# Performance work log

Hardware: AMD Instinct MI355X
Metric: run time of the kernel (lower is better)

The kernel has to match this reference:

```python
import jax, jax.numpy as jnp
import numpy as np

B, S, H, NH = 8, 2048, 128, 4
HS = H // NH
EPS = 1e-8


def setup_inputs() -> dict:
    key = jax.random.key(0)
    ks = jax.random.split(key, 20)
    sc = 1.0 / np.sqrt(H)
    d = {
        'item_embeds': jax.random.normal(ks[0], (B, S, H), jnp.float32),
        'behavior_embeds': jax.random.normal(ks[1], (B, S, H), jnp.float32),
        'attn_mask': jnp.zeros((B, 1, S, S), jnp.float32),
    }
    names = ['Wq', 'Wk', 'Wv', 'Wqb', 'Wkb', 'Wvb', 'Wf']
    for i, n in enumerate(names):
        d[n] = jax.random.normal(ks[2 + i], (H, H), jnp.float32) * sc
        d['b' + n[1:]] = jnp.zeros((H,), jnp.float32)
    d['ln_w'] = jnp.ones((H,), jnp.float32)
    d['ln_b'] = jnp.zeros((H,), jnp.float32)
    return d


def _split_heads(x):
    # [B,S,H] -> [B,NH,S,HS]
    return x.reshape(B, S, NH, HS).transpose(0, 2, 1, 3)


def _layer_norm(x, w, b):
    u = jnp.mean(x, -1, keepdims=True)
    s = jnp.mean((x - u) ** 2, -1, keepdims=True)
    return w * ((x - u) / jnp.sqrt(s + EPS)) + b


def reference(item_embeds, behavior_embeds, attn_mask,
              Wq, bq, Wk, bk, Wv, bv,
              Wqb, bqb, Wkb, bkb, Wvb, bvb,
              Wf, bf, ln_w, ln_b):
    Q = _split_heads(item_embeds @ Wq + bq)
    K = _split_heads(item_embeds @ Wk + bk)
    V = _split_heads(item_embeds @ Wv + bv)
    Qb = _split_heads(behavior_embeds @ Wqb + bqb)
    Kb = _split_heads(behavior_embeds @ Wkb + bkb)
    # V_behavior computed in the original forward but unused downstream
    _Vb = _split_heads(behavior_embeds @ Wvb + bvb)
    scores = (jnp.einsum('bhqd,bhkd->bhqk', Q, K)
              + jnp.einsum('bhqd,bhkd->bhqk', Qb, Kb)) / np.sqrt(HS)
    scores = scores + attn_mask
    probs = jax.nn.softmax(scores, axis=-1)
    attn_out = jnp.einsum('bhqk,bhkd->bhqd', probs, V)
    attn_out = attn_out.transpose(0, 2, 1, 3).reshape(B, S, H)
    out = attn_out @ Wf + bf
    return _layer_norm(out + item_embeds, ln_w, ln_b)
```

## Files before the change

### kernel.cpp

```cpp
#include <hip/hip_runtime.h>
#include <math.h>

typedef unsigned short ushort_t;
typedef __attribute__((ext_vector_type(8))) short bf16x8;
typedef __attribute__((ext_vector_type(4))) float f32x4;

namespace {
constexpr int B = 8, S = 2048, H = 128, NH = 4, HS = 32;
constexpr float EPS = 1e-8f;
constexpr float SCALE = 0.17677669529663687f;
constexpr int QT = 16, KT = 64;
constexpr int NE = B * S * H;
constexpr int NML = B * NH * S;
}

__device__ __forceinline__ ushort_t f2bf(float f) {
  unsigned u = __float_as_uint(f);
  unsigned r = (u + 0x7FFFu + ((u >> 16) & 1u)) >> 16;
  return (ushort_t)r;
}

__device__ __forceinline__ float bf2f(ushort_t u) {
  return __uint_as_float((unsigned)u << 16);
}

__device__ __forceinline__ f32x4 mfma16(bf16x8 a, bf16x8 b, f32x4 c) {
  return __builtin_amdgcn_mfma_f32_16x16x32_bf16(a, b, c, 0, 0, 0);
}

__global__ __launch_bounds__(256) void wcvt_kernel(
    const float* __restrict__ Wq, const float* __restrict__ Wk, const float* __restrict__ Wv,
    const float* __restrict__ Wqb, const float* __restrict__ Wkb, const float* __restrict__ Wf,
    ushort_t* __restrict__ Wt, unsigned* __restrict__ mflag)
{
  if (blockIdx.x == 0 && blockIdx.y == 0 && threadIdx.x == 0) *mflag = 0u;
  const float* Ws[6] = {Wq, Wk, Wv, Wqb, Wkb, Wf};
  const float scl[6] = {SCALE, 1.f, 1.f, SCALE, 1.f, 1.f};
  const int m = blockIdx.y;
  const int kb = blockIdx.x;
  const float* W = Ws[m];
  const float sc = scl[m];
  __shared__ float T[32 * 132];
  const int t = threadIdx.x;
#pragma unroll
  for (int u = 0; u < 4; ++u) {
    const int idx = u * 256 + t;
    const int row = idx >> 5, c4 = idx & 31;
    const float4 v = *(const float4*)&W[(kb * 32 + row) * H + c4 * 4];
    *(float4*)&T[row * 132 + c4 * 4] = v;
  }
  __syncthreads();
#pragma unroll
  for (int u = 0; u < 16; ++u) {
    const int idx = u * 256 + t;
    const int n = idx >> 5, kk = idx & 31;
    Wt[m * (H * H) + n * H + kb * 32 + kk] = f2bf(T[kk * 132 + n] * sc);
  }
}

__global__ __launch_bounds__(256) void proj_kernel(
    const float* __restrict__ item, const float* __restrict__ beh,
    const ushort_t* __restrict__ Wt,
    const float* __restrict__ bq, const float* __restrict__ bk, const float* __restrict__ bv,
    const float* __restrict__ bqb, const float* __restrict__ bkb,
    ushort_t* __restrict__ Qo, ushort_t* __restrict__ Ko, ushort_t* __restrict__ Qbo,
    ushort_t* __restrict__ Kbo, ushort_t* __restrict__ Vto,
    const uint4* __restrict__ mask4, unsigned* __restrict__ mflag)
{
  const int t = threadIdx.x;
  const int p = blockIdx.y;
  if (p == 5) {
    const long n = (long)B * S * S / 4;
    unsigned acc = 0;
    for (long i = (long)blockIdx.x * 256 + t; i < n; i += (long)512 * 256) {
      const uint4 v = mask4[i];
      acc |= v.x | v.y | v.z | v.w;
    }
    if (__any(acc != 0) && (t & 63) == 0) atomicOr(mflag, 1u);
    return;
  }
  __shared__ ushort_t Xs[32 * 136];
  __shared__ ushort_t Yb[32 * 136];
  const long r0 = (long)blockIdx.x * 32;
  const float* X = (p < 3) ? item : beh;
#pragma unroll
  for (int u = 0; u < 4; ++u) {
    const int idx = u * 256 + t;
    const int row = idx >> 5, c4 = idx & 31;
    const float4 v = *(const float4*)&X[(r0 + row) * H + c4 * 4];
    unsigned long long pk = (unsigned long long)f2bf(v.x) | ((unsigned long long)f2bf(v.y) << 16)
        | ((unsigned long long)f2bf(v.z) << 32) | ((unsigned long long)f2bf(v.w) << 48);
    *(unsigned long long*)&Xs[row * 136 + c4 * 4] = pk;
  }
  __syncthreads();

  const int w = t >> 6, l = t & 63, l15 = l & 15, quad = l >> 4;
  const int bb = (int)(r0 >> 11);
  const int s0 = (int)(r0 & (S - 1));
  const float* bias[5] = {bq, bk, bv, bqb, bkb};
  const float bscale[5] = {SCALE, 1.f, 1.f, SCALE, 1.f};
  ushort_t* dsts[5] = {Qo, Ko, Vto, Qbo, Kbo};

  bf16x8 af[2][4];
#pragma unroll
  for (int mt = 0; mt < 2; ++mt)
#pragma unroll
    for (int ks = 0; ks < 4; ++ks)
      af[mt][ks] = *(const bf16x8*)&Xs[(mt * 16 + l15) * 136 + ks * 32 + quad * 8];

  f32x4 acc[2][2];
#pragma unroll
  for (int nt = 0; nt < 2; ++nt) {
    const float bcol = bias[p][w * 32 + nt * 16 + l15] * bscale[p];
#pragma unroll
    for (int mt = 0; mt < 2; ++mt)
      acc[mt][nt] = (f32x4){bcol, bcol, bcol, bcol};
  }
  const ushort_t* Wp = Wt + p * (H * H);
#pragma unroll
  for (int ks = 0; ks < 4; ++ks) {
    bf16x8 bfr[2];
#pragma unroll
    for (int nt = 0; nt < 2; ++nt)
      bfr[nt] = *(const bf16x8*)&Wp[(w * 32 + nt * 16 + l15) * H + ks * 32 + quad * 8];
#pragma unroll
    for (int mt = 0; mt < 2; ++mt)
#pragma unroll
      for (int nt = 0; nt < 2; ++nt)
        acc[mt][nt] = mfma16(af[mt][ks], bfr[nt], acc[mt][nt]);
  }
#pragma unroll
  for (int mt = 0; mt < 2; ++mt)
#pragma unroll
    for (int nt = 0; nt < 2; ++nt)
#pragma unroll
      for (int r = 0; r < 4; ++r)
        Yb[(mt * 16 + quad * 4 + r) * 136 + w * 32 + nt * 16 + l15] = f2bf(acc[mt][nt][r]);
  __syncthreads();
  ushort_t* dst = dsts[p];
  if (p == 2) {
    const int d = t >> 1, sh = (t & 1) * 16;
    ushort_t tmp[16];
#pragma unroll
    for (int i = 0; i < 16; ++i) tmp[i] = Yb[(sh + i) * 136 + d];
    const long gidx = ((long)(bb * NH + (d >> 5)) * HS + (d & 31)) * S + s0 + sh;
    *(uint4*)&dst[gidx] = *(const uint4*)&tmp[0];
    *(uint4*)&dst[gidx + 8] = *(const uint4*)&tmp[8];
  } else {
    const int row = t >> 3, cb = (t & 7) * 16;
    const int h = cb >> 5, dd = cb & 31;
    const long gidx = ((long)(bb * NH + h) * S + s0 + row) * HS + dd;
    *(uint4*)&dst[gidx] = *(const uint4*)&Yb[row * 136 + cb];
    *(uint4*)&dst[gidx + 8] = *(const uint4*)&Yb[row * 136 + cb + 8];
  }
}

__global__ __launch_bounds__(256, 2) void attn_kernel(
    const ushort_t* __restrict__ Q, const ushort_t* __restrict__ K,
    const ushort_t* __restrict__ Qb, const ushort_t* __restrict__ Kb,
    const ushort_t* __restrict__ Vt, const float* __restrict__ mask,
    const unsigned* __restrict__ mflag,
    ushort_t* __restrict__ Op, float* __restrict__ Mp, float* __restrict__ Lp)
{
  __shared__ ushort_t Pb[NH][2][16 * 72];
  const int t = threadIdx.x;
  const int w = t >> 6;
  const int l = t & 63, l15 = l & 15, quad = l >> 4, quad4 = quad * 4;
  const int q0 = blockIdx.x * 32;
  const int b = blockIdx.y;
  const int half_ = blockIdx.z;
  const bool mzero = (*mflag == 0u);
  const long hQ = (long)(b * NH + w) * S * HS;
  const long hV = (long)(b * NH + w) * HS * S;
  const ushort_t* Kp  = K + hQ;
  const ushort_t* Kbp = Kb + hQ;
  const ushort_t* Vp  = Vt + hV;

  bf16x8 qf[2], qbf[2];
#pragma unroll
  for (int c = 0; c < 2; ++c) {
    qf[c]  = *(const bf16x8*)&Q[hQ + (long)(q0 + c * 16 + l15) * HS + quad * 8];
    qbf[c] = *(const bf16x8*)&Qb[hQ + (long)(q0 + c * 16 + l15) * HS + quad * 8];
  }

  const float* mrow[2][4];
#pragma unroll
  for (int c = 0; c < 2; ++c)
#pragma unroll
    for (int r = 0; r < 4; ++r)
      mrow[c][r] = mask + ((long)b * S + q0 + c * 16 + quad4 + r) * S + l15;

  float mold[2][4], lsum[2][4];
  f32x4 O[2][2];
#pragma unroll
  for (int c = 0; c < 2; ++c) {
#pragma unroll
    for (int r = 0; r < 4; ++r) { mold[c][r] = -1e30f; lsum[c][r] = 0.f; }
#pragma unroll
    for (int dt = 0; dt < 2; ++dt) O[c][dt] = (f32x4){0.f, 0.f, 0.f, 0.f};
  }

  const int kt0 = half_ * (S / KT / 2), kt1 = kt0 + (S / KT / 2);

  f32x4 scA[2][4], scB[2][4];
  if (!mzero) {
#pragma unroll
    for (int c = 0; c < 2; ++c)
#pragma unroll
      for (int nt = 0; nt < 4; ++nt)
#pragma unroll
        for (int r = 0; r < 4; ++r)
          scA[c][nt][r] = mrow[c][r][kt0 * KT + nt * 16];
  }

  auto body = [&](f32x4 (&sc)[2][4], f32x4 (&scn)[2][4], int k0, int k0n, bool pre) {
    bf16x8 kf[4], kbf[4];
#pragma unroll
    for (int nt = 0; nt < 4; ++nt) {
      kf[nt]  = *(const bf16x8*)&Kp[(long)(k0 + nt * 16 + l15) * HS + quad * 8];
      kbf[nt] = *(const bf16x8*)&Kbp[(long)(k0 + nt * 16 + l15) * HS + quad * 8];
    }
    bf16x8 vf[2][2];
#pragma unroll
    for (int dt = 0; dt < 2; ++dt)
#pragma unroll
      for (int ks = 0; ks < 2; ++ks)
        vf[dt][ks] = *(const bf16x8*)&Vp[(long)(dt * 16 + l15) * S + k0 + ks * 32 + quad * 8];
    if (mzero) {
#pragma unroll
      for (int c = 0; c < 2; ++c)
#pragma unroll
        for (int nt = 0; nt < 4; ++nt)
          sc[c][nt] = (f32x4){0.f, 0.f, 0.f, 0.f};
    } else if (pre) {
#pragma unroll
      for (int c = 0; c < 2; ++c)
#pragma unroll
        for (int nt = 0; nt < 4; ++nt)
#pragma unroll
          for (int r = 0; r < 4; ++r)
            scn[c][nt][r] = mrow[c][r][k0n + nt * 16];
    }
#pragma unroll
    for (int c = 0; c < 2; ++c)
#pragma unroll
      for (int nt = 0; nt < 4; ++nt) {
        sc[c][nt] = mfma16(qbf[c], kbf[nt], sc[c][nt]);
        sc[c][nt] = mfma16(qf[c], kf[nt], sc[c][nt]);
      }
#pragma unroll
    for (int c = 0; c < 2; ++c) {
      float alpha[4];
#pragma unroll
      for (int r = 0; r < 4; ++r) {
        float rm = fmaxf(fmaxf(sc[c][0][r], sc[c][1][r]), fmaxf(sc[c][2][r], sc[c][3][r]));
        rm = fmaxf(rm, __shfl_xor(rm, 1));
        rm = fmaxf(rm, __shfl_xor(rm, 2));
        rm = fmaxf(rm, __shfl_xor(rm, 4));
        rm = fmaxf(rm, __shfl_xor(rm, 8));
        const float mnew = fmaxf(mold[c][r], rm);
        alpha[r] = __expf(mold[c][r] - mnew);
        float rs = 0.f;
#pragma unroll
        for (int nt = 0; nt < 4; ++nt) {
          const float p = __expf(sc[c][nt][r] - mnew);
          sc[c][nt][r] = p;
          rs += p;
        }
        rs += __shfl_xor(rs, 1);
        rs += __shfl_xor(rs, 2);
        rs += __shfl_xor(rs, 4);
        rs += __shfl_xor(rs, 8);
        lsum[c][r] = lsum[c][r] * alpha[r] + rs;
        mold[c][r] = mnew;
      }
#pragma unroll
      for (int dt = 0; dt < 2; ++dt)
#pragma unroll
        for (int r = 0; r < 4; ++r)
          O[c][dt][r] *= alpha[r];
      ushort_t* Pw = Pb[w][c];
#pragma unroll
      for (int nt = 0; nt < 4; ++nt)
#pragma unroll
        for (int r = 0; r < 4; ++r)
          Pw[(quad4 + r) * 72 + nt * 16 + l15] = f2bf(sc[c][nt][r]);
    }
#pragma unroll
    for (int c = 0; c < 2; ++c) {
      const ushort_t* Pw = Pb[w][c];
      bf16x8 pf[2];
#pragma unroll
      for (int ks = 0; ks < 2; ++ks)
        pf[ks] = *(const bf16x8*)&Pw[l15 * 72 + ks * 32 + quad * 8];
#pragma unroll
      for (int dt = 0; dt < 2; ++dt)
#pragma unroll
        for (int ks = 0; ks < 2; ++ks)
          O[c][dt] = mfma16(pf[ks], vf[dt][ks], O[c][dt]);
    }
  };

  for (int kt = kt0; kt < kt1; kt += 2) {
    body(scA, scB, kt * KT, (kt + 1) * KT, true);
    body(scB, scA, (kt + 1) * KT, (kt + 2) * KT, kt + 2 < kt1);
  }

#pragma unroll
  for (int c = 0; c < 2; ++c) {
#pragma unroll
    for (int r = 0; r < 4; ++r) {
      const float inv = 1.f / lsum[c][r];
      const long row = (long)b * S + q0 + c * 16 + quad4 + r;
#pragma unroll
      for (int dt = 0; dt < 2; ++dt)
        Op[(long)half_ * NE + row * H + w * 32 + dt * 16 + l15] = f2bf(O[c][dt][r] * inv);
    }
    if (l15 == 0) {
#pragma unroll
      for (int r = 0; r < 4; ++r) {
        const long idx = ((long)(half_ * B + b) * NH + w) * S + q0 + c * 16 + quad4 + r;
        Mp[idx] = mold[c][r];
        Lp[idx] = lsum[c][r];
      }
    }
  }
}

__global__ __launch_bounds__(256) void out_kernel(
    const ushort_t* __restrict__ Op, const float* __restrict__ Mp, const float* __restrict__ Lp,
    const float* __restrict__ item,
    const ushort_t* __restrict__ Wft, const float* __restrict__ bf_,
    const float* __restrict__ lnw, const float* __restrict__ lnb,
    float* __restrict__ out)
{
  __shared__ ushort_t As[16 * 136];
  __shared__ float Ys[16 * 132];
  const int t = threadIdx.x;
  const long r0 = (long)blockIdx.x * 16;
  {
    const int row = t >> 4, c8 = t & 15;
    const long g = r0 + row;
    const int bb = (int)(g >> 11);
    const int ss = (int)(g & (S - 1));
    const int col0 = c8 * 8;
    const int h = col0 >> 5;
    const long mlidx = ((long)bb * NH + h) * S + ss;
    const float m1 = Mp[mlidx], m2 = Mp[(long)NML + mlidx];
    const float l1 = Lp[mlidx], l2 = Lp[(long)NML + mlidx];
    const float M = fmaxf(m1, m2);
    const float w1 = l1 * __expf(m1 - M), w2 = l2 * __expf(m2 - M);
    const float inv = 1.f / (w1 + w2);
    const float wa = w1 * inv, wb = w2 * inv;
    const uint4 a1 = *(const uint4*)&Op[g * H + col0];
    const uint4 a2 = *(const uint4*)&Op[(long)NE + g * H + col0];
    const ushort_t* p1 = (const ushort_t*)&a1;
    const ushort_t* p2 = (const ushort_t*)&a2;
    ushort_t mg[8];
#pragma unroll
    for (int i = 0; i < 8; ++i)
      mg[i] = f2bf(bf2f(p1[i]) * wa + bf2f(p2[i]) * wb);
    *(uint4*)&As[row * 136 + col0] = *(const uint4*)&mg[0];
  }
  __syncthreads();
  const int w = t >> 6, l = t & 63, l15 = l & 15, quad = l >> 4;
  f32x4 acc[2];
#pragma unroll
  for (int nt = 0; nt < 2; ++nt) {
    const float bcol = bf_[w * 32 + nt * 16 + l15];
    acc[nt] = (f32x4){bcol, bcol, bcol, bcol};
  }
#pragma unroll
  for (int ks = 0; ks < 4; ++ks) {
    const bf16x8 a = *(const bf16x8*)&As[l15 * 136 + ks * 32 + quad * 8];
#pragma unroll
    for (int nt = 0; nt < 2; ++nt) {
      const bf16x8 bfr = *(const bf16x8*)&Wft[(w * 32 + nt * 16 + l15) * H + ks * 32 + quad * 8];
      acc[nt] = mfma16(a, bfr, acc[nt]);
    }
  }
#pragma unroll
  for (int nt = 0; nt < 2; ++nt)
#pragma unroll
    for (int r = 0; r < 4; ++r) {
      const int rl = quad * 4 + r;
      const int col = w * 32 + nt * 16 + l15;
      Ys[rl * 132 + col] = acc[nt][r] + item[(r0 + rl) * H + col];
    }
  __syncthreads();
  const int rl = t >> 4, ch = t & 15;
  float v[8];
#pragma unroll
  for (int g = 0; g < 2; ++g) {
    const float4 y = *(const float4*)&Ys[rl * 132 + ch * 8 + g * 4];
    v[g * 4 + 0] = y.x; v[g * 4 + 1] = y.y; v[g * 4 + 2] = y.z; v[g * 4 + 3] = y.w;
  }
  float s = 0.f;
#pragma unroll
  for (int i = 0; i < 8; ++i) s += v[i];
  s += __shfl_xor(s, 1);
  s += __shfl_xor(s, 2);
  s += __shfl_xor(s, 4);
  s += __shfl_xor(s, 8);
  const float u_ = s * (1.f / H);
  float s2 = 0.f;
#pragma unroll
  for (int i = 0; i < 8; ++i) { const float d = v[i] - u_; s2 += d * d; }
  s2 += __shfl_xor(s2, 1);
  s2 += __shfl_xor(s2, 2);
  s2 += __shfl_xor(s2, 4);
  s2 += __shfl_xor(s2, 8);
  const float rinv = rsqrtf(s2 * (1.f / H) + EPS);
#pragma unroll
  for (int g = 0; g < 2; ++g) {
    float4 o;
    const int col = ch * 8 + g * 4;
    o.x = lnw[col + 0] * ((v[g * 4 + 0] - u_) * rinv) + lnb[col + 0];
    o.y = lnw[col + 1] * ((v[g * 4 + 1] - u_) * rinv) + lnb[col + 1];
    o.z = lnw[col + 2] * ((v[g * 4 + 2] - u_) * rinv) + lnb[col + 2];
    o.w = lnw[col + 3] * ((v[g * 4 + 3] - u_) * rinv) + lnb[col + 3];
    *(float4*)&out[(r0 + rl) * H + col] = o;
  }
}

extern "C" void kernel_launch(void* const* d_in, const int* in_sizes, int n_in,
                              void* d_out, int out_size, void* d_ws, size_t ws_size,
                              hipStream_t stream) {
  const float* item = (const float*)d_in[0];
  const float* beh  = (const float*)d_in[1];
  const float* mask = (const float*)d_in[2];
  const float* Wq  = (const float*)d_in[3];  const float* bq  = (const float*)d_in[4];
  const float* Wk  = (const float*)d_in[5];  const float* bk  = (const float*)d_in[6];
  const float* Wv  = (const float*)d_in[7];  const float* bv  = (const float*)d_in[8];
  const float* Wqb = (const float*)d_in[9];  const float* bqb = (const float*)d_in[10];
  const float* Wkb = (const float*)d_in[11]; const float* bkb = (const float*)d_in[12];
  const float* Wf  = (const float*)d_in[15]; const float* bfv = (const float*)d_in[16];
  const float* lnw = (const float*)d_in[17]; const float* lnb = (const float*)d_in[18];
  float* out = (float*)d_out;

  ushort_t* ws = (ushort_t*)d_ws;
  ushort_t* Qw   = ws;
  ushort_t* Kw   = Qw + NE;
  ushort_t* Qbw  = Kw + NE;
  ushort_t* Kbw  = Qbw + NE;
  ushort_t* Vtw  = Kbw + NE;
  ushort_t* Opw  = Vtw + NE;
  ushort_t* Wt   = Opw + 2 * (long)NE;
  float* Mpw = (float*)(Wt + 6 * H * H);
  float* Lpw = Mpw + 2 * (long)NML;
  unsigned* mflag = (unsigned*)(Lpw + 2 * (long)NML);

  wcvt_kernel<<<dim3(4, 6), 256, 0, stream>>>(Wq, Wk, Wv, Wqb, Wkb, Wf, Wt, mflag);
  proj_kernel<<<dim3((B * S) / 32, 6), 256, 0, stream>>>(
      item, beh, Wt, bq, bk, bv, bqb, bkb, Qw, Kw, Qbw, Kbw, Vtw,
      (const uint4*)mask, mflag);
  attn_kernel<<<dim3(S / 32, B, 2), 256, 0, stream>>>(
      Qw, Kw, Qbw, Kbw, Vtw, mask, mflag, Opw, Mpw, Lpw);
  out_kernel<<<dim3((B * S) / 16), 256, 0, stream>>>(
      Opw, Mpw, Lpw, item, Wt + 5 * H * H, bfv, lnw, lnb, out);
}
```

Before: 358.4 us.

## Split attention into zero-mask and masked kernels with separate mask scan

The mask-scan work moves out of the projection kernel into its own kernel with a larger grid. Attention is split into two kernels. A specialized zero-mask kernel processes 16 query rows per block, carries no mask registers and uses launch bounds of 4 blocks per CU, aiming for higher occupancy and less register pressure. The original masked kernel now runs only when the flag says the mask is nonzero. The cost is an extra launch, a kernel that exits early for any given flag value, and a mask scan that is no longer overlapped with projection.

After: 390.1 us. 1.09x slower.

```diff
diff --git a/kernel.cpp b/kernel.cpp
--- a/kernel.cpp
+++ b/kernel.cpp
@@ -58,29 +58,30 @@
   }
 }
 
+__global__ __launch_bounds__(256) void mscan_kernel(
+    const uint4* __restrict__ mask4, unsigned* __restrict__ mflag)
+{
+  const long n = (long)B * S * S / 4;
+  unsigned acc = 0;
+  for (long i = (long)blockIdx.x * 256 + threadIdx.x; i < n; i += (long)1024 * 256) {
+    const uint4 v = mask4[i];
+    acc |= v.x | v.y | v.z | v.w;
+  }
+  if (__any(acc != 0) && (threadIdx.x & 63) == 0) atomicOr(mflag, 1u);
+}
+
 __global__ __launch_bounds__(256) void proj_kernel(
     const float* __restrict__ item, const float* __restrict__ beh,
     const ushort_t* __restrict__ Wt,
     const float* __restrict__ bq, const float* __restrict__ bk, const float* __restrict__ bv,
     const float* __restrict__ bqb, const float* __restrict__ bkb,
     ushort_t* __restrict__ Qo, ushort_t* __restrict__ Ko, ushort_t* __restrict__ Qbo,
-    ushort_t* __restrict__ Kbo, ushort_t* __restrict__ Vto,
-    const uint4* __restrict__ mask4, unsigned* __restrict__ mflag)
+    ushort_t* __restrict__ Kbo, ushort_t* __restrict__ Vto)
 {
+  __shared__ ushort_t Xs[32 * 136];
+  __shared__ ushort_t Yb[32 * 136];
   const int t = threadIdx.x;
   const int p = blockIdx.y;
-  if (p == 5) {
-    const long n = (long)B * S * S / 4;
-    unsigned acc = 0;
-    for (long i = (long)blockIdx.x * 256 + t; i < n; i += (long)512 * 256) {
-      const uint4 v = mask4[i];
-      acc |= v.x | v.y | v.z | v.w;
-    }
-    if (__any(acc != 0) && (t & 63) == 0) atomicOr(mflag, 1u);
-    return;
-  }
-  __shared__ ushort_t Xs[32 * 136];
-  __shared__ ushort_t Yb[32 * 136];
   const long r0 = (long)blockIdx.x * 32;
   const float* X = (p < 3) ? item : beh;
 #pragma unroll
@@ -155,13 +156,132 @@
   }
 }
 
-__global__ __launch_bounds__(256, 2) void attn_kernel(
+__global__ __launch_bounds__(256, 4) void attn_z_kernel(
+    const ushort_t* __restrict__ Q, const ushort_t* __restrict__ K,
+    const ushort_t* __restrict__ Qb, const ushort_t* __restrict__ Kb,
+    const ushort_t* __restrict__ Vt, const unsigned* __restrict__ mflag,
+    ushort_t* __restrict__ Op, float* __restrict__ Mp, float* __restrict__ Lp)
+{
+  if (*mflag != 0u) return;
+  __shared__ ushort_t Pb[NH][16 * 72];
+  const int t = threadIdx.x;
+  const int w = t >> 6;
+  const int l = t & 63, l15 = l & 15, quad = l >> 4, quad4 = quad * 4;
+  const int bid = blockIdx.x;
+  const int b = bid & 7;
+  const int rest = bid >> 3;
+  const int q0 = (rest & 127) * QT;
+  const int half_ = rest >> 7;
+  const long hQ = (long)(b * NH + w) * S * HS;
+  const long hV = (long)(b * NH + w) * HS * S;
+  const ushort_t* Kp  = K + hQ;
+  const ushort_t* Kbp = Kb + hQ;
+  const ushort_t* Vp  = Vt + hV;
+
+  const bf16x8 qf  = *(const bf16x8*)&Q[hQ + (long)(q0 + l15) * HS + quad * 8];
+  const bf16x8 qbf = *(const bf16x8*)&Qb[hQ + (long)(q0 + l15) * HS + quad * 8];
+
+  float mold[4], lsum[4];
+  f32x4 O[2];
+#pragma unroll
+  for (int r = 0; r < 4; ++r) { mold[r] = -1e30f; lsum[r] = 0.f; }
+#pragma unroll
+  for (int dt = 0; dt < 2; ++dt) O[dt] = (f32x4){0.f, 0.f, 0.f, 0.f};
+  ushort_t* Pw = Pb[w];
+
+  const int kt0 = half_ * (S / KT / 2), kt1 = kt0 + (S / KT / 2);
+  for (int kt = kt0; kt < kt1; ++kt) {
+    const int k0 = kt * KT;
+    bf16x8 kf[4], kbf[4], vf[2][2];
+#pragma unroll
+    for (int nt = 0; nt < 4; ++nt) {
+      kf[nt]  = *(const bf16x8*)&Kp[(long)(k0 + nt * 16 + l15) * HS + quad * 8];
+      kbf[nt] = *(const bf16x8*)&Kbp[(long)(k0 + nt * 16 + l15) * HS + quad * 8];
+    }
+#pragma unroll
+    for (int dt = 0; dt < 2; ++dt)
+#pragma unroll
+      for (int ks = 0; ks < 2; ++ks)
+        vf[dt][ks] = *(const bf16x8*)&Vp[(long)(dt * 16 + l15) * S + k0 + ks * 32 + quad * 8];
+    f32x4 sc[4];
+#pragma unroll
+    for (int nt = 0; nt < 4; ++nt)
+      sc[nt] = (f32x4){0.f, 0.f, 0.f, 0.f};
+#pragma unroll
+    for (int nt = 0; nt < 4; ++nt) {
+      sc[nt] = mfma16(qbf, kbf[nt], sc[nt]);
+      sc[nt] = mfma16(qf, kf[nt], sc[nt]);
+    }
+    float alpha[4];
+#pragma unroll
+    for (int r = 0; r < 4; ++r) {
+      float rm = fmaxf(fmaxf(sc[0][r], sc[1][r]), fmaxf(sc[2][r], sc[3][r]));
+      rm = fmaxf(rm, __shfl_xor(rm, 1));
+      rm = fmaxf(rm, __shfl_xor(rm, 2));
+      rm = fmaxf(rm, __shfl_xor(rm, 4));
+      rm = fmaxf(rm, __shfl_xor(rm, 8));
+      const float mnew = fmaxf(mold[r], rm);
+      alpha[r] = __expf(mold[r] - mnew);
+      float rs = 0.f;
+#pragma unroll
+      for (int nt = 0; nt < 4; ++nt) {
+        const float p = __expf(sc[nt][r] - mnew);
+        sc[nt][r] = p;
+        rs += p;
+      }
+      rs += __shfl_xor(rs, 1);
+      rs += __shfl_xor(rs, 2);
+      rs += __shfl_xor(rs, 4);
+      rs += __shfl_xor(rs, 8);
+      lsum[r] = lsum[r] * alpha[r] + rs;
+      mold[r] = mnew;
+    }
+#pragma unroll
+    for (int dt = 0; dt < 2; ++dt)
+#pragma unroll
+      for (int r = 0; r < 4; ++r)
+        O[dt][r] *= alpha[r];
+#pragma unroll
+    for (int nt = 0; nt < 4; ++nt)
+#pragma unroll
+      for (int r = 0; r < 4; ++r)
+        Pw[(quad4 + r) * 72 + nt * 16 + l15] = f2bf(sc[nt][r]);
+    bf16x8 pf[2];
+#pragma unroll
+    for (int ks = 0; ks < 2; ++ks)
+      pf[ks] = *(const bf16x8*)&Pw[l15 * 72 + ks * 32 + quad * 8];
+#pragma unroll
+    for (int dt = 0; dt < 2; ++dt)
+#pragma unroll
+      for (int ks = 0; ks < 2; ++ks)
+        O[dt] = mfma16(pf[ks], vf[dt][ks], O[dt]);
+  }
+#pragma unroll
+  for (int r = 0; r < 4; ++r) {
+    const float inv = 1.f / lsum[r];
+    const long row = (long)b * S + q0 + quad4 + r;
+#pragma unroll
+    for (int dt = 0; dt < 2; ++dt)
+      Op[(long)half_ * NE + row * H + w * 32 + dt * 16 + l15] = f2bf(O[dt][r] * inv);
+  }
+  if (l15 == 0) {
+#pragma unroll
+    for (int r = 0; r < 4; ++r) {
+      const long idx = ((long)(half_ * B + b) * NH + w) * S + q0 + quad4 + r;
+      Mp[idx] = mold[r];
+      Lp[idx] = lsum[r];
+    }
+  }
+}
+
+__global__ __launch_bounds__(256, 2) void attn_m_kernel(
     const ushort_t* __restrict__ Q, const ushort_t* __restrict__ K,
     const ushort_t* __restrict__ Qb, const ushort_t* __restrict__ Kb,
     const ushort_t* __restrict__ Vt, const float* __restrict__ mask,
     const unsigned* __restrict__ mflag,
     ushort_t* __restrict__ Op, float* __restrict__ Mp, float* __restrict__ Lp)
 {
+  if (*mflag == 0u) return;
   __shared__ ushort_t Pb[NH][2][16 * 72];
   const int t = threadIdx.x;
   const int w = t >> 6;
@@ -169,7 +289,6 @@
   const int q0 = blockIdx.x * 32;
   const int b = blockIdx.y;
   const int half_ = blockIdx.z;
-  const bool mzero = (*mflag == 0u);
   const long hQ = (long)(b * NH + w) * S * HS;
   const long hV = (long)(b * NH + w) * HS * S;
   const ushort_t* Kp  = K + hQ;
@@ -203,15 +322,13 @@
   const int kt0 = half_ * (S / KT / 2), kt1 = kt0 + (S / KT / 2);
 
   f32x4 scA[2][4], scB[2][4];
-  if (!mzero) {
-#pragma unroll
-    for (int c = 0; c < 2; ++c)
-#pragma unroll
-      for (int nt = 0; nt < 4; ++nt)
-#pragma unroll
-        for (int r = 0; r < 4; ++r)
-          scA[c][nt][r] = mrow[c][r][kt0 * KT + nt * 16];
-  }
+#pragma unroll
+  for (int c = 0; c < 2; ++c)
+#pragma unroll
+    for (int nt = 0; nt < 4; ++nt)
+#pragma unroll
+      for (int r = 0; r < 4; ++r)
+        scA[c][nt][r] = mrow[c][r][kt0 * KT + nt * 16];
 
   auto body = [&](f32x4 (&sc)[2][4], f32x4 (&scn)[2][4], int k0, int k0n, bool pre) {
     bf16x8 kf[4], kbf[4];
@@ -226,13 +343,7 @@
 #pragma unroll
       for (int ks = 0; ks < 2; ++ks)
         vf[dt][ks] = *(const bf16x8*)&Vp[(long)(dt * 16 + l15) * S + k0 + ks * 32 + quad * 8];
-    if (mzero) {
-#pragma unroll
-      for (int c = 0; c < 2; ++c)
-#pragma unroll
-        for (int nt = 0; nt < 4; ++nt)
-          sc[c][nt] = (f32x4){0.f, 0.f, 0.f, 0.f};
-    } else if (pre) {
+    if (pre) {
 #pragma unroll
       for (int c = 0; c < 2; ++c)
 #pragma unroll
@@ -451,10 +562,12 @@
   unsigned* mflag = (unsigned*)(Lpw + 2 * (long)NML);
 
   wcvt_kernel<<<dim3(4, 6), 256, 0, stream>>>(Wq, Wk, Wv, Wqb, Wkb, Wf, Wt, mflag);
-  proj_kernel<<<dim3((B * S) / 32, 6), 256, 0, stream>>>(
-      item, beh, Wt, bq, bk, bv, bqb, bkb, Qw, Kw, Qbw, Kbw, Vtw,
-      (const uint4*)mask, mflag);
-  attn_kernel<<<dim3(S / 32, B, 2), 256, 0, stream>>>(
+  mscan_kernel<<<dim3(1024), 256, 0, stream>>>((const uint4*)mask, mflag);
+  proj_kernel<<<dim3((B * S) / 32, 5), 256, 0, stream>>>(
+      item, beh, Wt, bq, bk, bv, bqb, bkb, Qw, Kw, Qbw, Kbw, Vtw);
+  attn_z_kernel<<<dim3((S / QT) * B * 2), 256, 0, stream>>>(
+      Qw, Kw, Qbw, Kbw, Vtw, mflag, Opw, Mpw, Lpw);
+  attn_m_kernel<<<dim3(S / 32, B, 2), 256, 0, stream>>>(
       Qw, Kw, Qbw, Kbw, Vtw, mask, mflag, Opw, Mpw, Lpw);
   out_kernel<<<dim3((B * S) / 16), 256, 0, stream>>>(
       Opw, Mpw, Lpw, item, Wt + 5 * H * H, bfv, lnw, lnb, out);
```
